# Optimization experiments

Hardware: AMD Instinct MI355X
Metric: run time of the kernel (lower is better)

Reference implementation:

```python
import jax, jax.numpy as jnp
import numpy as np

NBR_SIZE = 3
ALPHA = -1.0
EPS = 1e-12  # torch F.normalize eps


def _l2norm(x, axis):
    n = jnp.sqrt(jnp.sum(x * x, axis=axis, keepdims=True))
    return x / jnp.maximum(n, EPS)


def setup_inputs() -> dict:
    key = jax.random.key(0)
    k1, k2 = jax.random.split(key)
    nbrs = jax.random.normal(k1, (4, 4, 64, 128, 128), dtype=jnp.float32)  # [b, n_frames, c, h, w]
    ref = jax.random.normal(k2, (4, 64, 128, 128), dtype=jnp.float32)      # [b, c, h, w]
    return {"nbrs": nbrs, "ref": ref}


def reference(nbrs, ref):
    b, n, c, h, w = nbrs.shape
    pad = NBR_SIZE // 2
    # mean over neighbor frames, detached in the original
    mean = jax.lax.stop_gradient(jnp.mean(nbrs, axis=1))          # [b,c,h,w]
    # ref is detached+cloned before normalization in the original
    ref_n = _l2norm(jax.lax.stop_gradient(ref), axis=1)           # [b,c,h,w], unit-norm over c

    outs = []
    for i in range(n):  # small fixed number of frames
        nbr = nbrs[:, i]                                          # [b,c,h,w]
        wdiff = jnp.exp(ALPHA * (nbr - mean) ** 2)                # [b,c,h,w]
        p = jnp.pad(nbr, ((0, 0), (0, 0), (pad, pad), (pad, pad)), mode='reflect')
        # unfold: k2 = NBR_SIZE**2 shifted views -> [b,c,k2,h,w]
        win = jnp.stack([p[:, :, dy:dy + h, dx:dx + w]
                         for dy in range(NBR_SIZE) for dx in range(NBR_SIZE)], axis=2)
        win_n = _l2norm(win, axis=1)                              # normalize over channels
        # per-pixel cosine similarity: [b,k2,h,w]
        d = jnp.einsum('bchw,bckhw->bkhw', ref_n, win_n)
        wt = jax.nn.softmax(d, axis=1)                            # softmax over k2 window positions
        # aggregate normalized window features: [b,c,h,w]
        agg = jnp.einsum('bkhw,bckhw->bchw', wt, win_n)
        outs.append(agg * wdiff)

    return jnp.stack(outs + [ref], axis=1)                        # [b, n+1, c, h, w]
```

## Files before the change

### kernel.cpp

```cpp
#include <hip/hip_runtime.h>
#include <math.h>

namespace {

constexpr int B_ = 4, N_ = 4, C_ = 64, H_ = 128, W_ = 128;
constexpr int HW_ = H_ * W_;

__global__ __launch_bounds__(256) void copyref_kernel(const float* __restrict__ ref,
                                                      float* __restrict__ out) {
    int t = blockIdx.x * 256 + threadIdx.x;
    int f = t * 4;
    int b = f / (C_ * HW_);
    int within = f - b * (C_ * HW_);
    float4 v = *reinterpret_cast<const float4*>(ref + (size_t)b * C_ * HW_ + within);
    *reinterpret_cast<float4*>(out + (size_t)(b * 5 + N_) * C_ * HW_ + within) = v;
}

__global__ __launch_bounds__(256) void localcorr_kernel(const float* __restrict__ nbrs,
                                                        const float* __restrict__ ref,
                                                        float* __restrict__ out) {
    __shared__ float s_own[2][4][128];
    __shared__ float s_nrm[4][128];

    const int blk = blockIdx.x;
    const int ypair = blk & 63;
    const int bi = blk >> 6;
    const int i = bi & 3;
    const int b = bi >> 2;
    const int t = (int)threadIdx.x;
    const int x = t & 127;
    const int ry = t >> 7;
    const int y0 = ypair * 2;
    const int y = y0 + ry;

    const int xm = (x == 0) ? 1 : x - 1;
    const int xp = (x == W_ - 1) ? W_ - 2 : x + 1;
    const int gyA = (y0 == 0) ? 1 : y0 - 1;
    const int gyB = y0;
    const int gyC = y0 + 1;
    const int gyD = (y0 + 2 == H_) ? H_ - 2 : y0 + 2;
    const int myRowA = (ry == 0) ? gyA : gyC;
    const int myRowB = (ry == 0) ? gyB : gyD;

    const float* __restrict__ nb = nbrs + (size_t)(b * N_ + i) * C_ * HW_;
    const float* __restrict__ rp = ref + (size_t)b * C_ * HW_;
    const int offA = myRowA * W_ + x;
    const int offB = myRowB * W_ + x;
    const int offR = y * W_ + x;

    float dot[9];
#pragma unroll
    for (int k = 0; k < 9; ++k) dot[k] = 0.f;
    float nA = 0.f, nB = 0.f, r2 = 0.f;

    float o0 = nb[offA], o1 = nb[offB], rf = rp[offR];
#pragma unroll 1
    for (int c = 0; c < C_; ++c) {
        const int cur = c & 1;
        s_own[cur][2 * ry + 0][x] = o0;
        s_own[cur][2 * ry + 1][x] = o1;
        float o0n = 0.f, o1n = 0.f, rfn = 0.f;
        if (c + 1 < C_) {
            const size_t co = (size_t)(c + 1) * HW_;
            o0n = nb[co + offA];
            o1n = nb[co + offB];
            rfn = rp[co + offR];
        }
        __syncthreads();
        const float w00 = s_own[cur][ry + 0][xm], w02 = s_own[cur][ry + 0][xp];
        const float w10 = s_own[cur][ry + 1][xm], w12 = s_own[cur][ry + 1][xp];
        const float w20 = s_own[cur][ry + 2][xm], w22 = s_own[cur][ry + 2][xp];
        float w01, w11, w21;
        if (ry == 0) { w01 = o0; w11 = o1; w21 = s_own[cur][2][x]; }
        else         { w01 = s_own[cur][1][x]; w11 = o0; w21 = o1; }
        nA += o0 * o0; nB += o1 * o1; r2 += rf * rf;
        dot[0] += rf * w00; dot[1] += rf * w01; dot[2] += rf * w02;
        dot[3] += rf * w10; dot[4] += rf * w11; dot[5] += rf * w12;
        dot[6] += rf * w20; dot[7] += rf * w21; dot[8] += rf * w22;
        o0 = o0n; o1 = o1n; rf = rfn;
    }

    s_nrm[2 * ry + 0][x] = nA;
    s_nrm[2 * ry + 1][x] = nB;
    __syncthreads();
    float nk[9];
    nk[0] = s_nrm[ry + 0][xm]; nk[1] = s_nrm[ry + 0][x]; nk[2] = s_nrm[ry + 0][xp];
    nk[3] = s_nrm[ry + 1][xm]; nk[4] = s_nrm[ry + 1][x]; nk[5] = s_nrm[ry + 1][xp];
    nk[6] = s_nrm[ry + 2][xm]; nk[7] = s_nrm[ry + 2][x]; nk[8] = s_nrm[ry + 2][xp];

    const float invr = rsqrtf(fmaxf(r2, 1e-24f));
    float inv[9], d[9];
#pragma unroll
    for (int k = 0; k < 9; ++k) {
        inv[k] = rsqrtf(fmaxf(nk[k], 1e-24f));
        d[k] = dot[k] * invr * inv[k];
    }
    float mx = d[0];
#pragma unroll
    for (int k = 1; k < 9; ++k) mx = fmaxf(mx, d[k]);
    float ssum = 0.f;
#pragma unroll
    for (int k = 0; k < 9; ++k) { d[k] = __expf(d[k] - mx); ssum += d[k]; }
    const float is = 1.f / ssum;
    float wtp[9];
#pragma unroll
    for (int k = 0; k < 9; ++k) wtp[k] = d[k] * is * inv[k];

    const float* __restrict__ pm0 = nbrs + (size_t)(b * N_ + ((i + 1) & 3)) * C_ * HW_;
    const float* __restrict__ pm1 = nbrs + (size_t)(b * N_ + ((i + 2) & 3)) * C_ * HW_;
    const float* __restrict__ pm2 = nbrs + (size_t)(b * N_ + ((i + 3) & 3)) * C_ * HW_;
    float* __restrict__ op = out + (size_t)(b * 5 + i) * C_ * HW_ + offR;

    o0 = nb[offA]; o1 = nb[offB];
    float q0 = pm0[offR], q1 = pm1[offR], q2 = pm2[offR];
#pragma unroll 1
    for (int c = 0; c < C_; ++c) {
        const int cur = c & 1;
        s_own[cur][2 * ry + 0][x] = o0;
        s_own[cur][2 * ry + 1][x] = o1;
        float o0n = 0.f, o1n = 0.f, q0n = 0.f, q1n = 0.f, q2n = 0.f;
        if (c + 1 < C_) {
            const size_t co = (size_t)(c + 1) * HW_;
            o0n = nb[co + offA];
            o1n = nb[co + offB];
            q0n = pm0[co + offR];
            q1n = pm1[co + offR];
            q2n = pm2[co + offR];
        }
        __syncthreads();
        const float w00 = s_own[cur][ry + 0][xm], w02 = s_own[cur][ry + 0][xp];
        const float w10 = s_own[cur][ry + 1][xm], w12 = s_own[cur][ry + 1][xp];
        const float w20 = s_own[cur][ry + 2][xm], w22 = s_own[cur][ry + 2][xp];
        float w01, w11, w21;
        if (ry == 0) { w01 = o0; w11 = o1; w21 = s_own[cur][2][x]; }
        else         { w01 = s_own[cur][1][x]; w11 = o0; w21 = o1; }
        const float agg = wtp[0] * w00 + wtp[1] * w01 + wtp[2] * w02
                        + wtp[3] * w10 + wtp[4] * w11 + wtp[5] * w12
                        + wtp[6] * w20 + wtp[7] * w21 + wtp[8] * w22;
        const float ctr = w11;
        const float dd = ctr - 0.25f * (ctr + q0 + q1 + q2);
        op[(size_t)c * HW_] = agg * __expf(-dd * dd);
        o0 = o0n; o1 = o1n; q0 = q0n; q1 = q1n; q2 = q2n;
    }
}

}

extern "C" void kernel_launch(void* const* d_in, const int* in_sizes, int n_in,
                              void* d_out, int out_size, void* d_ws, size_t ws_size,
                              hipStream_t stream) {
    const float* nbrs = (const float*)d_in[0];
    const float* ref = (const float*)d_in[1];
    float* out = (float*)d_out;

    copyref_kernel<<<(B_ * C_ * HW_ / 4) / 256, 256, 0, stream>>>(ref, out);

    localcorr_kernel<<<B_ * N_ * (H_ / 2), 256, 0, stream>>>(nbrs, ref, out);
}
```

Baseline: 81.35 us.

## Replace shared-memory stencil exchange with direct cached global loads

```diff
diff --git a/kernel.cpp b/kernel.cpp
--- a/kernel.cpp
+++ b/kernel.cpp
@@ -19,9 +19,6 @@
 __global__ __launch_bounds__(256) void localcorr_kernel(const float* __restrict__ nbrs,
                                                         const float* __restrict__ ref,
                                                         float* __restrict__ out) {
-    __shared__ float s_own[2][4][128];
-    __shared__ float s_nrm[4][128];
-
     const int blk = blockIdx.x;
     const int ypair = blk & 63;
     const int bi = blk >> 6;
@@ -30,117 +27,78 @@
     const int t = (int)threadIdx.x;
     const int x = t & 127;
     const int ry = t >> 7;
-    const int y0 = ypair * 2;
-    const int y = y0 + ry;
+    const int y = ypair * 2 + ry;
 
-    const int xm = (x == 0) ? 1 : x - 1;
-    const int xp = (x == W_ - 1) ? W_ - 2 : x + 1;
-    const int gyA = (y0 == 0) ? 1 : y0 - 1;
-    const int gyB = y0;
-    const int gyC = y0 + 1;
-    const int gyD = (y0 + 2 == H_) ? H_ - 2 : y0 + 2;
-    const int myRowA = (ry == 0) ? gyA : gyC;
-    const int myRowB = (ry == 0) ? gyB : gyD;
+    const int xm1 = (x == 0) ? 1 : x - 1;
+    const int xp1 = (x == W_ - 1) ? W_ - 2 : x + 1;
+    const int ym1 = (y == 0) ? 1 : y - 1;
+    const int yp1 = (y == H_ - 1) ? H_ - 2 : y + 1;
+
+    const int ro0 = ym1 * W_, ro1 = y * W_, ro2 = yp1 * W_;
+    const int offR = y * W_ + x;
 
     const float* __restrict__ nb = nbrs + (size_t)(b * N_ + i) * C_ * HW_;
     const float* __restrict__ rp = ref + (size_t)b * C_ * HW_;
-    const int offA = myRowA * W_ + x;
-    const int offB = myRowB * W_ + x;
-    const int offR = y * W_ + x;
 
-    float dot[9];
+    float dot[9], nrm[9];
 #pragma unroll
-    for (int k = 0; k < 9; ++k) dot[k] = 0.f;
-    float nA = 0.f, nB = 0.f, r2 = 0.f;
+    for (int k = 0; k < 9; ++k) { dot[k] = 0.f; nrm[k] = 0.f; }
+    float r2 = 0.f;
 
-    float o0 = nb[offA], o1 = nb[offB], rf = rp[offR];
-#pragma unroll 1
+#pragma unroll 4
     for (int c = 0; c < C_; ++c) {
-        const int cur = c & 1;
-        s_own[cur][2 * ry + 0][x] = o0;
-        s_own[cur][2 * ry + 1][x] = o1;
-        float o0n = 0.f, o1n = 0.f, rfn = 0.f;
-        if (c + 1 < C_) {
-            const size_t co = (size_t)(c + 1) * HW_;
-            o0n = nb[co + offA];
-            o1n = nb[co + offB];
-            rfn = rp[co + offR];
-        }
-        __syncthreads();
-        const float w00 = s_own[cur][ry + 0][xm], w02 = s_own[cur][ry + 0][xp];
-        const float w10 = s_own[cur][ry + 1][xm], w12 = s_own[cur][ry + 1][xp];
-        const float w20 = s_own[cur][ry + 2][xm], w22 = s_own[cur][ry + 2][xp];
-        float w01, w11, w21;
-        if (ry == 0) { w01 = o0; w11 = o1; w21 = s_own[cur][2][x]; }
-        else         { w01 = s_own[cur][1][x]; w11 = o0; w21 = o1; }
-        nA += o0 * o0; nB += o1 * o1; r2 += rf * rf;
+        const float* pc = nb + (size_t)c * HW_;
+        const float w00 = pc[ro0 + xm1], w01 = pc[ro0 + x], w02 = pc[ro0 + xp1];
+        const float w10 = pc[ro1 + xm1], w11 = pc[ro1 + x], w12 = pc[ro1 + xp1];
+        const float w20 = pc[ro2 + xm1], w21 = pc[ro2 + x], w22 = pc[ro2 + xp1];
+        const float rf = rp[(size_t)c * HW_ + offR];
+        r2 += rf * rf;
+        nrm[0] += w00 * w00; nrm[1] += w01 * w01; nrm[2] += w02 * w02;
+        nrm[3] += w10 * w10; nrm[4] += w11 * w11; nrm[5] += w12 * w12;
+        nrm[6] += w20 * w20; nrm[7] += w21 * w21; nrm[8] += w22 * w22;
         dot[0] += rf * w00; dot[1] += rf * w01; dot[2] += rf * w02;
         dot[3] += rf * w10; dot[4] += rf * w11; dot[5] += rf * w12;
         dot[6] += rf * w20; dot[7] += rf * w21; dot[8] += rf * w22;
-        o0 = o0n; o1 = o1n; rf = rfn;
     }
 
-    s_nrm[2 * ry + 0][x] = nA;
-    s_nrm[2 * ry + 1][x] = nB;
-    __syncthreads();
-    float nk[9];
-    nk[0] = s_nrm[ry + 0][xm]; nk[1] = s_nrm[ry + 0][x]; nk[2] = s_nrm[ry + 0][xp];
-    nk[3] = s_nrm[ry + 1][xm]; nk[4] = s_nrm[ry + 1][x]; nk[5] = s_nrm[ry + 1][xp];
-    nk[6] = s_nrm[ry + 2][xm]; nk[7] = s_nrm[ry + 2][x]; nk[8] = s_nrm[ry + 2][xp];
-
     const float invr = rsqrtf(fmaxf(r2, 1e-24f));
-    float inv[9], d[9];
+    float iv[9], d[9];
 #pragma unroll
     for (int k = 0; k < 9; ++k) {
-        inv[k] = rsqrtf(fmaxf(nk[k], 1e-24f));
-        d[k] = dot[k] * invr * inv[k];
+        iv[k] = rsqrtf(fmaxf(nrm[k], 1e-24f));
+        d[k] = dot[k] * invr * iv[k];
     }
     float mx = d[0];
 #pragma unroll
     for (int k = 1; k < 9; ++k) mx = fmaxf(mx, d[k]);
-    float ssum = 0.f;
+    float ss = 0.f;
 #pragma unroll
-    for (int k = 0; k < 9; ++k) { d[k] = __expf(d[k] - mx); ssum += d[k]; }
-    const float is = 1.f / ssum;
+    for (int k = 0; k < 9; ++k) { d[k] = __expf(d[k] - mx); ss += d[k]; }
+    const float is = 1.f / ss;
     float wtp[9];
 #pragma unroll
-    for (int k = 0; k < 9; ++k) wtp[k] = d[k] * is * inv[k];
+    for (int k = 0; k < 9; ++k) wtp[k] = d[k] * is * iv[k];
 
     const float* __restrict__ pm0 = nbrs + (size_t)(b * N_ + ((i + 1) & 3)) * C_ * HW_;
     const float* __restrict__ pm1 = nbrs + (size_t)(b * N_ + ((i + 2) & 3)) * C_ * HW_;
     const float* __restrict__ pm2 = nbrs + (size_t)(b * N_ + ((i + 3) & 3)) * C_ * HW_;
     float* __restrict__ op = out + (size_t)(b * 5 + i) * C_ * HW_ + offR;
 
-    o0 = nb[offA]; o1 = nb[offB];
-    float q0 = pm0[offR], q1 = pm1[offR], q2 = pm2[offR];
-#pragma unroll 1
+#pragma unroll 4
     for (int c = 0; c < C_; ++c) {
-        const int cur = c & 1;
-        s_own[cur][2 * ry + 0][x] = o0;
-        s_own[cur][2 * ry + 1][x] = o1;
-        float o0n = 0.f, o1n = 0.f, q0n = 0.f, q1n = 0.f, q2n = 0.f;
-        if (c + 1 < C_) {
-            const size_t co = (size_t)(c + 1) * HW_;
-            o0n = nb[co + offA];
-            o1n = nb[co + offB];
-            q0n = pm0[co + offR];
-            q1n = pm1[co + offR];
-            q2n = pm2[co + offR];
-        }
-        __syncthreads();
-        const float w00 = s_own[cur][ry + 0][xm], w02 = s_own[cur][ry + 0][xp];
-        const float w10 = s_own[cur][ry + 1][xm], w12 = s_own[cur][ry + 1][xp];
-        const float w20 = s_own[cur][ry + 2][xm], w22 = s_own[cur][ry + 2][xp];
-        float w01, w11, w21;
-        if (ry == 0) { w01 = o0; w11 = o1; w21 = s_own[cur][2][x]; }
-        else         { w01 = s_own[cur][1][x]; w11 = o0; w21 = o1; }
+        const float* pc = nb + (size_t)c * HW_;
+        const float w00 = pc[ro0 + xm1], w01 = pc[ro0 + x], w02 = pc[ro0 + xp1];
+        const float w10 = pc[ro1 + xm1], w11 = pc[ro1 + x], w12 = pc[ro1 + xp1];
+        const float w20 = pc[ro2 + xm1], w21 = pc[ro2 + x], w22 = pc[ro2 + xp1];
+        const float q0 = pm0[(size_t)c * HW_ + offR];
+        const float q1 = pm1[(size_t)c * HW_ + offR];
+        const float q2 = pm2[(size_t)c * HW_ + offR];
         const float agg = wtp[0] * w00 + wtp[1] * w01 + wtp[2] * w02
                         + wtp[3] * w10 + wtp[4] * w11 + wtp[5] * w12
                         + wtp[6] * w20 + wtp[7] * w21 + wtp[8] * w22;
         const float ctr = w11;
         const float dd = ctr - 0.25f * (ctr + q0 + q1 + q2);
         op[(size_t)c * HW_] = agg * __expf(-dd * dd);
-        o0 = o0n; o1 = o1n; q0 = q0n; q1 = q1n; q2 = q2n;
     }
 }
 
```

New measurement: 95.14 us. +17.0%, slower.
